# Performance work log

Hardware: AMD Instinct MI355X
Metric: run time of the kernel (lower is better)

Reference implementation:

```python
import jax, jax.numpy as jnp
import numpy as np

N, E, F, H, G = 50000, 800000, 64, 64, 100

def setup_inputs() -> dict:
    key = jax.random.key(0)
    ks = jax.random.split(key, 12)
    x = jax.random.normal(ks[0], (N, F), dtype=jnp.float32)
    edge_index = jax.random.randint(ks[1], (2, E), 0, N, dtype=jnp.int64)
    batch = jnp.sort(jax.random.randint(ks[2], (N,), 0, G, dtype=jnp.int64))
    s1 = 1.0 / np.sqrt(F); s2 = 1.0 / np.sqrt(H)
    W1 = jax.random.normal(ks[3], (2, F, H), dtype=jnp.float32) * s1
    b1 = jnp.zeros((H,), dtype=jnp.float32)
    W2 = jax.random.normal(ks[4], (2, H, H), dtype=jnp.float32) * s2
    b2 = jnp.zeros((H,), dtype=jnp.float32)
    gamma = jnp.ones((H,), dtype=jnp.float32)
    beta = jnp.zeros((H,), dtype=jnp.float32)
    linW = jax.random.normal(ks[5], (H, 1), dtype=jnp.float32) * s2
    linb = jnp.zeros((1,), dtype=jnp.float32)
    return {"x": x, "edge_index": edge_index, "batch": batch, "W1": W1, "b1": b1,
            "W2": W2, "b2": b2, "gamma": gamma, "beta": beta, "linW": linW, "linb": linb}

def _edge_norm(row, col, n):
    # get_laplacian(sym) + lambda_max=2: Lhat off-diag weight = -d_i^{-1/2} d_j^{-1/2}, diag = 0
    deg = jax.ops.segment_sum(jnp.ones(row.shape[0], jnp.float32), row, num_segments=n)
    dis = jnp.where(deg > 0, deg ** -0.5, 0.0)
    return -dis[row] * dis[col]

def _cheb(x, row, col, w, W, b):
    # K=2: out = T0(Lhat)x @ W0 + T1(Lhat)x @ W1 + b, T1 = Lhat x via scatter-add
    Tx1 = jax.ops.segment_sum(w[:, None] * x[row], col, num_segments=x.shape[0])
    return x @ W[0] + Tx1 @ W[1] + b

def reference(x, edge_index, batch, W1, b1, W2, b2, gamma, beta, linW, linb):
    row, col = edge_index[0], edge_index[1]
    n = x.shape[0]
    w = _edge_norm(row, col, n)
    h = _cheb(x, row, col, w, W1, b1)
    # BatchNorm1d (training-mode batch stats, eps=1e-5)
    mu = jnp.mean(h, axis=0)
    var = jnp.var(h, axis=0)
    h = (h - mu) * jax.lax.rsqrt(var + 1e-5) * gamma + beta
    # LeakyReLU (default slope 0.01)
    h = jnp.where(h >= 0, h, 0.01 * h)
    h = _cheb(h, row, col, w, W2, b2)
    # global_mean_pool over graph ids
    sums = jax.ops.segment_sum(h, batch, num_segments=G)
    cnts = jax.ops.segment_sum(jnp.ones(n, jnp.float32), batch, num_segments=G)
    pooled = sums / jnp.maximum(cnts, 1.0)[:, None]
    # dropout: identity (eval)
    return pooled @ linW + linb
```

## Files before the change

### kernel.cpp

```cpp
#include <hip/hip_runtime.h>

#define HDIM 64
#define BH 128
#define HB8 12800
#define SBINS 12544
#define GR 32


__device__ __forceinline__ int lbound(const int* __restrict__ b, int n, int v) {
    int lo = 0, hi = n;
    while (lo < hi) { int m = (lo + hi) >> 1; if (b[m] < v) lo = m + 1; else hi = m; }
    return lo;
}

__device__ __forceinline__ unsigned short f2bf(float f) {
    unsigned u = __float_as_uint(f);
    unsigned r = u + 0x7FFFu + ((u >> 16) & 1u);
    return (unsigned short)(r >> 16);
}


__global__ __launch_bounds__(256) void k_hist8(const int* __restrict__ row,
                                               const int* __restrict__ col,
                                               unsigned char* __restrict__ cntP,
                                               unsigned char* __restrict__ degP,
                                               int E, int N, int slice) {
    __shared__ unsigned hbin[HB8];
    int blk = blockIdx.x;
    const int* keys = blockIdx.y ? row : col;
    unsigned char* outP = blockIdx.y ? degP : cntP;
    int binsU = (N + 3) >> 2;
    for (int i = threadIdx.x; i < binsU; i += 256) hbin[i] = 0;
    __syncthreads();
    int e0 = blk * slice, e1 = min(e0 + slice, E);
    for (int e = e0 + threadIdx.x; e < e1; e += 256) {
        int c = keys[e];
        atomicAdd(&hbin[c >> 2], 1u << ((c & 3) << 3));
    }
    __syncthreads();
    unsigned* outU = (unsigned*)(outP + (size_t)blk * N);
    for (int i = threadIdx.x; i < binsU; i += 256) outU[i] = hbin[i];
}

__global__ void k_prefA(unsigned char* __restrict__ cntP,
                        const unsigned char* __restrict__ degP,
                        int* __restrict__ cnt, float* __restrict__ dis, int N) {
    int i = blockIdx.x * blockDim.x + threadIdx.x;
    if (i >= N) return;
    int run = 0;
    #pragma unroll 4
    for (int b = 0; b < BH; ++b) {
        int v = cntP[(size_t)b * N + i];
        cntP[(size_t)b * N + i] = (unsigned char)run;
        run += v;
    }
    cnt[i] = run;
    int d = 0;
    #pragma unroll 4
    for (int b = 0; b < BH; ++b) d += degP[(size_t)b * N + i];
    dis[i] = d > 0 ? rsqrtf((float)d) : 0.0f;
}

__global__ __launch_bounds__(1024) void k_scan1(const int* __restrict__ cnt,
                                                int* __restrict__ start,
                                                int* __restrict__ bsum, int n) {
    __shared__ int wsum[16];
    int i = blockIdx.x * 1024 + threadIdx.x;
    int lane = threadIdx.x & 63, w = threadIdx.x >> 6;
    int v = (i < n) ? cnt[i] : 0;
    int incl = v;
    #pragma unroll
    for (int off = 1; off < 64; off <<= 1) {
        int u = __shfl_up(incl, off, 64);
        if (lane >= off) incl += u;
    }
    if (lane == 63) wsum[w] = incl;
    __syncthreads();
    if (w == 0) {
        int s = (lane < 16) ? wsum[lane] : 0;
        int si = s;
        #pragma unroll
        for (int off = 1; off < 16; off <<= 1) {
            int u = __shfl_up(si, off, 64);
            if (lane >= off) si += u;
        }
        if (lane < 16) wsum[lane] = si - s;
    }
    __syncthreads();
    int excl = incl - v + wsum[w];
    if (i < n) start[i] = excl;
    if (threadIdx.x == 1023) bsum[blockIdx.x] = excl + v;
}

__global__ void k_scan2(int* __restrict__ bsum, int nb) {
    int lane = threadIdx.x;
    if (lane >= 64) return;
    int v = (lane < nb) ? bsum[lane] : 0;
    int incl = v;
    #pragma unroll
    for (int off = 1; off < 64; off <<= 1) {
        int u = __shfl_up(incl, off, 64);
        if (lane >= off) incl += u;
    }
    if (lane < nb) bsum[lane] = incl - v;
}

__global__ void k_scan3(int* __restrict__ start, const int* __restrict__ bsum, int n) {
    int i = blockIdx.x * blockDim.x + threadIdx.x;
    if (i < n) start[i] += bsum[i >> 10];
}

__global__ __launch_bounds__(256) void k_sortfill(const int* __restrict__ row,
                                                  const int* __restrict__ col,
                                                  const unsigned char* __restrict__ cntP,
                                                  const int* __restrict__ start,
                                                  int* __restrict__ er,
                                                  int E, int N, int slice) {
    __shared__ int cur[SBINS];
    int blk = blockIdx.x;
    int lo = blockIdx.y * SBINS;
    int span = min(SBINS, N - lo);
    for (int i = threadIdx.x; i < span; i += 256)
        cur[i] = start[lo + i] + (int)cntP[(size_t)blk * N + lo + i];
    __syncthreads();
    int e0 = blk * slice, e1 = min(e0 + slice, E);
    for (int e = e0 + threadIdx.x; e < e1; e += 256) {
        int c = col[e] - lo;
        int rv = row[e];
        if ((unsigned)c < (unsigned)span) {
            int pos = atomicAdd(&cur[c], 1);
            er[pos] = rv;
        }
    }
}


__global__ __launch_bounds__(512) void k_gemm2(const float* __restrict__ x,
                                               const float* __restrict__ dis,
                                               const float* __restrict__ W1,
                                               const float* __restrict__ b1,
                                               float* __restrict__ z,
                                               unsigned short* __restrict__ y16, int n) {
    __shared__ float xs[GR][HDIM];
    int tid  = threadIdx.x;
    int j    = tid & 63;
    int half = (tid >> 6) & 1;
    int w2   = tid >> 7;
    int base = blockIdx.x * GR;

    const float* Wb = W1 + (half ? HDIM * HDIM : 0);
    float4 wr[16];
    #pragma unroll
    for (int k4 = 0; k4 < 16; ++k4) {
        wr[k4].x = Wb[(k4 * 4 + 0) * HDIM + j];
        wr[k4].y = Wb[(k4 * 4 + 1) * HDIM + j];
        wr[k4].z = Wb[(k4 * 4 + 2) * HDIM + j];
        wr[k4].w = Wb[(k4 * 4 + 3) * HDIM + j];
    }
    float bj = b1[j];

    {
        int v = tid;
        int r = base + (v >> 4);
        int rc = min(r, n - 1);
        int c = (v & 15) * 4;
        ((float4*)xs)[v] = *(const float4*)&x[(size_t)rc * HDIM + c];
    }
    __syncthreads();

    #pragma unroll
    for (int m = 0; m < 8; ++m) {
        int lr = w2 * 8 + m;
        int r = base + lr;
        if (r < n) {
            const float4* rp = (const float4*)xs[lr];
            float a = 0.f;
            #pragma unroll
            for (int k4 = 0; k4 < 16; ++k4) {
                float4 v = rp[k4];
                a = fmaf(v.x, wr[k4].x, a);
                a = fmaf(v.y, wr[k4].y, a);
                a = fmaf(v.z, wr[k4].z, a);
                a = fmaf(v.w, wr[k4].w, a);
            }
            if (half == 0) z[(size_t)r * HDIM + j] = a + bj;
            else           y16[(size_t)r * HDIM + j] = f2bf(dis[r] * a);
        }
    }
}

__global__ __launch_bounds__(256) void k_gatherH(const int* __restrict__ er,
                                                 const int* __restrict__ start,
                                                 const int* __restrict__ cnt,
                                                 const float* __restrict__ dis,
                                                 const unsigned* __restrict__ y32,
                                                 const float* __restrict__ z,
                                                 float* __restrict__ h,
                                                 float* __restrict__ pstat, int n) {
    __shared__ float red[2][4][HDIM];
    int w = threadIdx.x >> 6;
    int lane = threadIdx.x & 63;
    int l  = lane & 31;
    int hi = lane >> 5;
    float sx = 0.f, sy = 0.f, qx = 0.f, qy = 0.f;
    #pragma unroll
    for (int m = 0; m < 4; ++m) {
        int i = blockIdx.x * 16 + w * 4 + m;
        if (i >= n) continue;
        int s = start[i], nd = cnt[i];
        float a0x = 0.f, a0y = 0.f, a1x = 0.f, a1y = 0.f;
        int k = 0;
        for (; k + 3 < nd; k += 4) {
            int r0 = er[s + k + hi];
            int r1 = er[s + k + 2 + hi];
            unsigned v0 = y32[(size_t)r0 * 32 + l];
            unsigned v1 = y32[(size_t)r1 * 32 + l];
            a0x += __uint_as_float(v0 << 16);
            a0y += __uint_as_float(v0 & 0xFFFF0000u);
            a1x += __uint_as_float(v1 << 16);
            a1y += __uint_as_float(v1 & 0xFFFF0000u);
        }
        for (; k < nd; k += 2) {
            int idx = k + hi;
            if (idx < nd) {
                unsigned v = y32[(size_t)er[s + idx] * 32 + l];
                a0x += __uint_as_float(v << 16);
                a0y += __uint_as_float(v & 0xFFFF0000u);
            }
        }
        float ax = a0x + a1x, ay = a0y + a1y;
        ax += __shfl_xor(ax, 32, 64);
        ay += __shfl_xor(ay, 32, 64);
        if (hi == 0) {
            float di = dis[i];
            float2 zv = *(const float2*)&z[(size_t)i * HDIM + 2 * l];
            float h0 = zv.x - di * ax;
            float h1 = zv.y - di * ay;
            *(float2*)&h[(size_t)i * HDIM + 2 * l] = make_float2(h0, h1);
            sx += h0; sy += h1;
            qx = fmaf(h0, h0, qx); qy = fmaf(h1, h1, qy);
        }
    }
    if (hi == 0) {
        *(float2*)&red[0][w][2 * l] = make_float2(sx, sy);
        *(float2*)&red[1][w][2 * l] = make_float2(qx, qy);
    }
    __syncthreads();
    if (w == 0) {
        int j = lane;
        float s  = red[0][0][j] + red[0][1][j] + red[0][2][j] + red[0][3][j];
        float ss = red[1][0][j] + red[1][1][j] + red[1][2][j] + red[1][3][j];
        pstat[(size_t)blockIdx.x * 128 + j]      = s;
        pstat[(size_t)blockIdx.x * 128 + 64 + j] = ss;
    }
}

__global__ __launch_bounds__(256) void k_statred(const float* __restrict__ pstat,
                                                 float* __restrict__ stats, int nb) {
    int idx = blockIdx.x;
    float s = 0.f;
    for (int b = threadIdx.x; b < nb; b += 256)
        s += pstat[(size_t)b * 128 + idx];
    __shared__ float red[256];
    red[threadIdx.x] = s;
    __syncthreads();
    for (int off = 128; off > 0; off >>= 1) {
        if (threadIdx.x < off) red[threadIdx.x] += red[threadIdx.x + off];
        __syncthreads();
    }
    if (threadIdx.x == 0) stats[idx] = red[0];
}

__global__ void k_prep(const float* __restrict__ stats,
                       const float* __restrict__ gamma, const float* __restrict__ beta,
                       const float* __restrict__ W2, const float* __restrict__ b2,
                       const float* __restrict__ linW, const float* __restrict__ linb,
                       float* __restrict__ scale, float* __restrict__ shift,
                       float* __restrict__ u0, float* __restrict__ u1,
                       float* __restrict__ c0, int n) {
    int k = threadIdx.x;
    if (k >= HDIM) return;
    float inv_n = 1.0f / (float)n;
    float mu  = stats[k] * inv_n;
    float var = stats[64 + k] * inv_n - mu * mu;
    float rs  = rsqrtf(var + 1e-5f);
    float sc  = rs * gamma[k];
    scale[k] = sc;
    shift[k] = beta[k] - mu * sc;
    float a0 = 0.f, a1 = 0.f;
    #pragma unroll 8
    for (int j = 0; j < HDIM; ++j) {
        float lw = linW[j];
        a0 = fmaf(W2[k * HDIM + j], lw, a0);
        a1 = fmaf(W2[HDIM * HDIM + k * HDIM + j], lw, a1);
    }
    u0[k] = a0;
    u1[k] = a1;
    if (k == 0) {
        float c = linb[0];
        for (int j = 0; j < HDIM; ++j) c = fmaf(b2[j], linW[j], c);
        c0[0] = c;
    }
}

__global__ __launch_bounds__(256) void k_node(const float* __restrict__ h,
                                              const float* __restrict__ scale,
                                              const float* __restrict__ shift,
                                              const float* __restrict__ u0,
                                              const float* __restrict__ u1,
                                              const float* __restrict__ dis,
                                              float* __restrict__ a, float* __restrict__ t,
                                              int n) {
    int i = blockIdx.x * 4 + (threadIdx.x >> 6);
    if (i >= n) return;
    int j = threadIdx.x & 63;
    float v = fmaf(h[(size_t)i * HDIM + j], scale[j], shift[j]);
    v = v >= 0.f ? v : 0.01f * v;
    float p0 = v * u0[j];
    float p1 = v * u1[j];
    #pragma unroll
    for (int off = 32; off > 0; off >>= 1) {
        p0 += __shfl_xor(p0, off, 64);
        p1 += __shfl_xor(p1, off, 64);
    }
    if (j == 0) { a[i] = p0; t[i] = dis[i] * p1; }
}

__global__ void k_gather2(const int* __restrict__ er, const int* __restrict__ start,
                          const int* __restrict__ cnt, const float* __restrict__ dis,
                          const float* __restrict__ t, const float* __restrict__ a,
                          float* __restrict__ s2, int n) {
    int i = blockIdx.x * blockDim.x + threadIdx.x;
    if (i >= n) return;
    int s = start[i], nd = cnt[i];
    float s0 = 0.f, s1 = 0.f, s2v = 0.f, s3 = 0.f;
    int k = 0;
    for (; k + 3 < nd; k += 4) {
        s0 += t[er[s + k]];
        s1 += t[er[s + k + 1]];
        s2v += t[er[s + k + 2]];
        s3 += t[er[s + k + 3]];
    }
    for (; k < nd; ++k) s0 += t[er[s + k]];
    s2[i] = a[i] - dis[i] * ((s0 + s1) + (s2v + s3));
}

__global__ __launch_bounds__(256) void k_pool2(const float* __restrict__ s2,
                                               const int* __restrict__ batch,
                                               const float* __restrict__ c0,
                                               const float* __restrict__ linb,
                                               float* __restrict__ out, int n) {
    int g = blockIdx.x;
    int lo = lbound(batch, n, g);
    int hi = lbound(batch, n, g + 1);
    float s = 0.f;
    for (int i = lo + threadIdx.x; i < hi; i += 256) s += s2[i];
    __shared__ float red[256];
    red[threadIdx.x] = s;
    __syncthreads();
    for (int off = 128; off > 0; off >>= 1) {
        if (threadIdx.x < off) red[threadIdx.x] += red[threadIdx.x + off];
        __syncthreads();
    }
    if (threadIdx.x == 0) {
        int cntg = hi - lo;
        out[g] = cntg > 0 ? red[0] / (float)cntg + c0[0] : linb[0];
    }
}


extern "C" void kernel_launch(void* const* d_in, const int* in_sizes, int n_in,
                              void* d_out, int out_size, void* d_ws, size_t ws_size,
                              hipStream_t stream) {
    const float* x     = (const float*)d_in[0];
    const int*   eidx  = (const int*)d_in[1];
    const int*   batch = (const int*)d_in[2];
    const float* W1    = (const float*)d_in[3];
    const float* b1    = (const float*)d_in[4];
    const float* W2    = (const float*)d_in[5];
    const float* b2    = (const float*)d_in[6];
    const float* gamma = (const float*)d_in[7];
    const float* beta  = (const float*)d_in[8];
    const float* linW  = (const float*)d_in[9];
    const float* linb  = (const float*)d_in[10];
    float* out = (float*)d_out;

    const int N = in_sizes[0] / HDIM;
    const int E = in_sizes[1] / 2;
    const int G = out_size;
    const int NB = (N + 1023) / 1024;
    const int slice = (E + BH - 1) / BH;
    const int NHB = (N + 15) / 16;

    const int* row = eidx;
    const int* col = eidx + E;

    char* wsb = (char*)d_ws;
    float* h    = (float*)wsb;               wsb += (size_t)N * HDIM * 4;
    unsigned char* cntP = (unsigned char*)h;
    unsigned char* degP = cntP + (size_t)BH * N;
    float* z    = (float*)wsb;               wsb += (size_t)N * HDIM * 4;
    unsigned short* y16 = (unsigned short*)wsb; wsb += (size_t)N * HDIM * 2;
    int*   cnt   = (int*)wsb;                wsb += (size_t)N * 4;
    int*   start = (int*)wsb;                wsb += (size_t)N * 4;
    int*   bsum  = (int*)wsb;                wsb += (size_t)NB * 4 + 64;
    int*   er    = (int*)wsb;                wsb += (size_t)E * 4;
    float* dis   = (float*)wsb;              wsb += (size_t)N * 4;
    float* a     = (float*)wsb;              wsb += (size_t)N * 4;
    float* t     = (float*)wsb;              wsb += (size_t)N * 4;
    float* s2    = (float*)wsb;              wsb += (size_t)N * 4;
    float* pstat = (float*)wsb;              wsb += (size_t)NHB * 128 * 4;
    float* stats = (float*)wsb;              wsb += 128 * 4;
    float* scale = (float*)wsb;              wsb += HDIM * 4;
    float* shift = (float*)wsb;              wsb += HDIM * 4;
    float* u0    = (float*)wsb;              wsb += HDIM * 4;
    float* u1    = (float*)wsb;              wsb += HDIM * 4;
    float* c0    = (float*)wsb;              wsb += 64;

    k_hist8<<<dim3(BH, 2), 256, 0, stream>>>(row, col, cntP, degP, E, N, slice);
    k_prefA<<<(N + 255) / 256, 256, 0, stream>>>(cntP, degP, cnt, dis, N);
    k_scan1<<<NB, 1024, 0, stream>>>(cnt, start, bsum, N);
    k_scan2<<<1, 64, 0, stream>>>(bsum, NB);
    k_scan3<<<(N + 255) / 256, 256, 0, stream>>>(start, bsum, N);
    k_sortfill<<<dim3(BH, 4), 256, 0, stream>>>(row, col, cntP, start, er, E, N, slice);
    k_gemm2<<<(N + GR - 1) / GR, 512, 0, stream>>>(x, dis, W1, b1, z, y16, N);
    k_gatherH<<<NHB, 256, 0, stream>>>(er, start, cnt, dis, (const unsigned*)y16, z,
                                       h, pstat, N);
    k_statred<<<128, 256, 0, stream>>>(pstat, stats, NHB);
    k_prep<<<1, 64, 0, stream>>>(stats, gamma, beta, W2, b2, linW, linb,
                                 scale, shift, u0, u1, c0, N);
    k_node<<<(N + 3) / 4, 256, 0, stream>>>(h, scale, shift, u0, u1, dis, a, t, N);
    k_gather2<<<(N + 255) / 256, 256, 0, stream>>>(er, start, cnt, dis, t, a, s2, N);
    k_pool2<<<G, 256, 0, stream>>>(s2, batch, c0, linb, out, N);
}
```

Before: 173.5 us.

## Fuse CSR metadata scan, narrow edge indices to 16-bit, fuse gather2 with pooling

Merges the per-node prefix, degree computation and the three-pass scan into one kernel that uses a decoupled lookback over per-block aggregates. Edge source indices and counts are stored as 16-bit values to halve gather index traffic. The second gather is fused with graph mean pooling through shared and global atomics, plus a tiny output kernel. The aim is fewer launches and less memory traffic. The 16-bit indices only hold for N below 65536, and the lookback spin-wait relies on earlier blocks being resident so they can make progress.

```diff
diff --git a/kernel.cpp b/kernel.cpp
--- a/kernel.cpp
+++ b/kernel.cpp
@@ -42,33 +42,31 @@
     for (int i = threadIdx.x; i < binsU; i += 256) outU[i] = hbin[i];
 }
 
-__global__ void k_prefA(unsigned char* __restrict__ cntP,
-                        const unsigned char* __restrict__ degP,
-                        int* __restrict__ cnt, float* __restrict__ dis, int N) {
-    int i = blockIdx.x * blockDim.x + threadIdx.x;
-    if (i >= N) return;
-    int run = 0;
-    #pragma unroll 4
-    for (int b = 0; b < BH; ++b) {
-        int v = cntP[(size_t)b * N + i];
-        cntP[(size_t)b * N + i] = (unsigned char)run;
-        run += v;
-    }
-    cnt[i] = run;
-    int d = 0;
-    #pragma unroll 4
-    for (int b = 0; b < BH; ++b) d += degP[(size_t)b * N + i];
-    dis[i] = d > 0 ? rsqrtf((float)d) : 0.0f;
-}
-
-__global__ __launch_bounds__(1024) void k_scan1(const int* __restrict__ cnt,
-                                                int* __restrict__ start,
-                                                int* __restrict__ bsum, int n) {
+__global__ __launch_bounds__(1024) void k_csrmeta(unsigned char* __restrict__ cntP,
+                                                  const unsigned char* __restrict__ degP,
+                                                  unsigned short* __restrict__ cnt16,
+                                                  float* __restrict__ dis,
+                                                  int* __restrict__ start,
+                                                  int* __restrict__ agg, int N) {
     __shared__ int wsum[16];
+    __shared__ int sTotal, sBase;
     int i = blockIdx.x * 1024 + threadIdx.x;
     int lane = threadIdx.x & 63, w = threadIdx.x >> 6;
-    int v = (i < n) ? cnt[i] : 0;
-    int incl = v;
+
+    int run = 0, d = 0;
+    if (i < N) {
+        #pragma unroll 4
+        for (int b = 0; b < BH; ++b) {
+            int v = cntP[(size_t)b * N + i];
+            cntP[(size_t)b * N + i] = (unsigned char)run;
+            run += v;
+        }
+        #pragma unroll 4
+        for (int b = 0; b < BH; ++b) d += degP[(size_t)b * N + i];
+        cnt16[i] = (unsigned short)run;
+        dis[i] = d > 0 ? rsqrtf((float)d) : 0.0f;
+    }
+    int incl = run;
     #pragma unroll
     for (int off = 1; off < 64; off <<= 1) {
         int u = __shfl_up(incl, off, 64);
@@ -87,34 +85,35 @@
         if (lane < 16) wsum[lane] = si - s;
     }
     __syncthreads();
-    int excl = incl - v + wsum[w];
-    if (i < n) start[i] = excl;
-    if (threadIdx.x == 1023) bsum[blockIdx.x] = excl + v;
-}
-
-__global__ void k_scan2(int* __restrict__ bsum, int nb) {
-    int lane = threadIdx.x;
-    if (lane >= 64) return;
-    int v = (lane < nb) ? bsum[lane] : 0;
-    int incl = v;
-    #pragma unroll
-    for (int off = 1; off < 64; off <<= 1) {
-        int u = __shfl_up(incl, off, 64);
-        if (lane >= off) incl += u;
-    }
-    if (lane < nb) bsum[lane] = incl - v;
-}
-
-__global__ void k_scan3(int* __restrict__ start, const int* __restrict__ bsum, int n) {
-    int i = blockIdx.x * blockDim.x + threadIdx.x;
-    if (i < n) start[i] += bsum[i >> 10];
+    int excl = incl - run + wsum[w];
+    if (threadIdx.x == 1023) sTotal = excl + run;
+    __syncthreads();
+    if (threadIdx.x == 0)
+        __hip_atomic_store(&agg[blockIdx.x], sTotal + 1,
+                           __ATOMIC_RELEASE, __HIP_MEMORY_SCOPE_AGENT);
+    if (w == 0) {
+        int v = 0;
+        if (lane < (int)blockIdx.x) {
+            int a;
+            do {
+                a = __hip_atomic_load(&agg[lane], __ATOMIC_ACQUIRE,
+                                      __HIP_MEMORY_SCOPE_AGENT);
+            } while (a == 0);
+            v = a - 1;
+        }
+        #pragma unroll
+        for (int off = 1; off < 64; off <<= 1) v += __shfl_xor(v, off, 64);
+        if (lane == 0) sBase = v;
+    }
+    __syncthreads();
+    if (i < N) start[i] = excl + sBase;
 }
 
 __global__ __launch_bounds__(256) void k_sortfill(const int* __restrict__ row,
                                                   const int* __restrict__ col,
                                                   const unsigned char* __restrict__ cntP,
                                                   const int* __restrict__ start,
-                                                  int* __restrict__ er,
+                                                  unsigned short* __restrict__ er,
                                                   int E, int N, int slice) {
     __shared__ int cur[SBINS];
     int blk = blockIdx.x;
@@ -129,7 +128,7 @@
         int rv = row[e];
         if ((unsigned)c < (unsigned)span) {
             int pos = atomicAdd(&cur[c], 1);
-            er[pos] = rv;
+            er[pos] = (unsigned short)rv;
         }
     }
 }
@@ -189,9 +188,9 @@
     }
 }
 
-__global__ __launch_bounds__(256) void k_gatherH(const int* __restrict__ er,
+__global__ __launch_bounds__(256) void k_gatherH(const unsigned short* __restrict__ er,
                                                  const int* __restrict__ start,
-                                                 const int* __restrict__ cnt,
+                                                 const unsigned short* __restrict__ cnt16,
                                                  const float* __restrict__ dis,
                                                  const unsigned* __restrict__ y32,
                                                  const float* __restrict__ z,
@@ -207,7 +206,7 @@
     for (int m = 0; m < 4; ++m) {
         int i = blockIdx.x * 16 + w * 4 + m;
         if (i >= n) continue;
-        int s = start[i], nd = cnt[i];
+        int s = start[i], nd = cnt16[i];
         float a0x = 0.f, a0y = 0.f, a1x = 0.f, a1y = 0.f;
         int k = 0;
         for (; k + 3 < nd; k += 4) {
@@ -326,45 +325,53 @@
     if (j == 0) { a[i] = p0; t[i] = dis[i] * p1; }
 }
 
-__global__ void k_gather2(const int* __restrict__ er, const int* __restrict__ start,
-                          const int* __restrict__ cnt, const float* __restrict__ dis,
-                          const float* __restrict__ t, const float* __restrict__ a,
-                          float* __restrict__ s2, int n) {
+__global__ __launch_bounds__(256) void k_gp(const unsigned short* __restrict__ er,
+                                            const int* __restrict__ start,
+                                            const unsigned short* __restrict__ cnt16,
+                                            const float* __restrict__ dis,
+                                            const float* __restrict__ t,
+                                            const float* __restrict__ a,
+                                            const int* __restrict__ batch,
+                                            float* __restrict__ gsum, int n) {
+    __shared__ float gacc[16];
+    __shared__ int sGmin;
+    int tid = threadIdx.x;
+    int i = (int)blockIdx.x * 64 + (tid >> 2);
+    int q = tid & 3;
+    if (tid < 16) gacc[tid] = 0.f;
+    if (tid == 0) sGmin = batch[min((int)blockIdx.x * 64, n - 1)];
+    __syncthreads();
+    if (i < n) {
+        int s = start[i], nd = cnt16[i];
+        float acc = 0.f;
+        int k = q;
+        for (; k + 4 < nd; k += 8) {
+            acc += t[er[s + k]] + t[er[s + k + 4]];
+        }
+        if (k < nd) acc += t[er[s + k]];
+        acc += __shfl_xor(acc, 1, 4);
+        acc += __shfl_xor(acc, 2, 4);
+        if (q == 0) {
+            float s2 = a[i] - dis[i] * acc;
+            int g = batch[i];
+            int rel = g - sGmin;
+            if ((unsigned)rel < 16u) atomicAdd(&gacc[rel], s2);
+            else                     atomicAdd(&gsum[g], s2);
+        }
+    }
+    __syncthreads();
+    if (tid < 16 && gacc[tid] != 0.f) atomicAdd(&gsum[sGmin + tid], gacc[tid]);
+}
+
+__global__ void k_out(const float* __restrict__ gsum, const int* __restrict__ batch,
+                      const float* __restrict__ c0, const float* __restrict__ linb,
+                      float* __restrict__ out, int n, int g) {
     int i = blockIdx.x * blockDim.x + threadIdx.x;
-    if (i >= n) return;
-    int s = start[i], nd = cnt[i];
-    float s0 = 0.f, s1 = 0.f, s2v = 0.f, s3 = 0.f;
-    int k = 0;
-    for (; k + 3 < nd; k += 4) {
-        s0 += t[er[s + k]];
-        s1 += t[er[s + k + 1]];
-        s2v += t[er[s + k + 2]];
-        s3 += t[er[s + k + 3]];
-    }
-    for (; k < nd; ++k) s0 += t[er[s + k]];
-    s2[i] = a[i] - dis[i] * ((s0 + s1) + (s2v + s3));
-}
-
-__global__ __launch_bounds__(256) void k_pool2(const float* __restrict__ s2,
-                                               const int* __restrict__ batch,
-                                               const float* __restrict__ c0,
-                                               const float* __restrict__ linb,
-                                               float* __restrict__ out, int n) {
-    int g = blockIdx.x;
-    int lo = lbound(batch, n, g);
-    int hi = lbound(batch, n, g + 1);
-    float s = 0.f;
-    for (int i = lo + threadIdx.x; i < hi; i += 256) s += s2[i];
-    __shared__ float red[256];
-    red[threadIdx.x] = s;
-    __syncthreads();
-    for (int off = 128; off > 0; off >>= 1) {
-        if (threadIdx.x < off) red[threadIdx.x] += red[threadIdx.x + off];
-        __syncthreads();
-    }
-    if (threadIdx.x == 0) {
-        int cntg = hi - lo;
-        out[g] = cntg > 0 ? red[0] / (float)cntg + c0[0] : linb[0];
+    if (i < g) {
+        int lo = lbound(batch, n, i);
+        int hi = lbound(batch, n, i + 1);
+        int c = hi - lo;
+        out[i] = c > 0 ? gsum[i] / (float)c + c0[0] : linb[0];
     }
 }
 
@@ -401,15 +408,15 @@
     unsigned char* degP = cntP + (size_t)BH * N;
     float* z    = (float*)wsb;               wsb += (size_t)N * HDIM * 4;
     unsigned short* y16 = (unsigned short*)wsb; wsb += (size_t)N * HDIM * 2;
-    int*   cnt   = (int*)wsb;                wsb += (size_t)N * 4;
+    unsigned short* cnt16 = (unsigned short*)wsb; wsb += (size_t)N * 2;
+    unsigned short* er    = (unsigned short*)wsb; wsb += (size_t)E * 2;
     int*   start = (int*)wsb;                wsb += (size_t)N * 4;
-    int*   bsum  = (int*)wsb;                wsb += (size_t)NB * 4 + 64;
-    int*   er    = (int*)wsb;                wsb += (size_t)E * 4;
     float* dis   = (float*)wsb;              wsb += (size_t)N * 4;
     float* a     = (float*)wsb;              wsb += (size_t)N * 4;
     float* t     = (float*)wsb;              wsb += (size_t)N * 4;
-    float* s2    = (float*)wsb;              wsb += (size_t)N * 4;
     float* pstat = (float*)wsb;              wsb += (size_t)NHB * 128 * 4;
+    int*   agg   = (int*)wsb;                wsb += 64 * 4;
+    float* gsum  = (float*)wsb;              wsb += 128 * 4;
     float* stats = (float*)wsb;              wsb += 128 * 4;
     float* scale = (float*)wsb;              wsb += HDIM * 4;
     float* shift = (float*)wsb;              wsb += HDIM * 4;
@@ -417,19 +424,18 @@
     float* u1    = (float*)wsb;              wsb += HDIM * 4;
     float* c0    = (float*)wsb;              wsb += 64;
 
+    (void)hipMemsetAsync(agg, 0, (64 + 128) * 4, stream);
+
     k_hist8<<<dim3(BH, 2), 256, 0, stream>>>(row, col, cntP, degP, E, N, slice);
-    k_prefA<<<(N + 255) / 256, 256, 0, stream>>>(cntP, degP, cnt, dis, N);
-    k_scan1<<<NB, 1024, 0, stream>>>(cnt, start, bsum, N);
-    k_scan2<<<1, 64, 0, stream>>>(bsum, NB);
-    k_scan3<<<(N + 255) / 256, 256, 0, stream>>>(start, bsum, N);
+    k_csrmeta<<<NB, 1024, 0, stream>>>(cntP, degP, cnt16, dis, start, agg, N);
     k_sortfill<<<dim3(BH, 4), 256, 0, stream>>>(row, col, cntP, start, er, E, N, slice);
     k_gemm2<<<(N + GR - 1) / GR, 512, 0, stream>>>(x, dis, W1, b1, z, y16, N);
-    k_gatherH<<<NHB, 256, 0, stream>>>(er, start, cnt, dis, (const unsigned*)y16, z,
+    k_gatherH<<<NHB, 256, 0, stream>>>(er, start, cnt16, dis, (const unsigned*)y16, z,
                                        h, pstat, N);
     k_statred<<<128, 256, 0, stream>>>(pstat, stats, NHB);
     k_prep<<<1, 64, 0, stream>>>(stats, gamma, beta, W2, b2, linW, linb,
                                  scale, shift, u0, u1, c0, N);
     k_node<<<(N + 3) / 4, 256, 0, stream>>>(h, scale, shift, u0, u1, dis, a, t, N);
-    k_gather2<<<(N + 255) / 256, 256, 0, stream>>>(er, start, cnt, dis, t, a, s2, N);
-    k_pool2<<<G, 256, 0, stream>>>(s2, batch, c0, linb, out, N);
-}
+    k_gp<<<(N + 63) / 64, 256, 0, stream>>>(er, start, cnt16, dis, t, a, batch, gsum, N);
+    k_out<<<1, 128, 0, stream>>>(gsum, batch, c0, linb, out, N, G);
+}
```

After: 177.3 us. 2.2% more time.
